# Performance work log

Hardware: AMD Instinct MI355X
Metric: run time of the kernel (lower is better)

Reference implementation:

```python
import jax, jax.numpy as jnp
import numpy as np

PATCH = 3
SIGMA2 = 0.5 ** 2
EPS = 1e-8


def _gauss_kernel():
    # depthwise Gaussian patch kernel, shape (6, 1, P, P, P), normalized to sum 1
    c = (PATCH - 1) / 2.0
    zz, yy, xx = np.meshgrid(np.arange(PATCH), np.arange(PATCH), np.arange(PATCH), indexing='ij')
    d2 = (xx - c) ** 2 + (yy - c) ** 2 + (zz - c) ** 2
    g = np.exp(-d2 / SIGMA2).astype(np.float32)
    g /= g.sum()
    k = np.zeros((6, 1, PATCH, PATCH, PATCH), np.float32)
    k[:, 0] = g
    return jnp.asarray(k)


def _shift(x, axis, step):
    # zero-padded shift: step=+1 -> out[i] = x[i+1]; step=-1 -> out[i] = x[i-1]
    n = x.shape[axis]
    pad = [(0, 0)] * x.ndim
    lo = 1 if step > 0 else 0
    pad[axis] = (0, 1) if step > 0 else (1, 0)
    xp = jnp.pad(x, pad)
    idx = [slice(None)] * x.ndim
    idx[axis] = slice(lo, lo + n)
    return xp[tuple(idx)]


def _mind(img):
    # shift-conv (one-hot 3x3x3 kernels) == 6 axis shifts: +z,-z,+y,-y,+x,-x
    shifted = jnp.concatenate([
        _shift(img, 2, 1), _shift(img, 2, -1),
        _shift(img, 3, 1), _shift(img, 3, -1),
        _shift(img, 4, 1), _shift(img, 4, -1),
    ], axis=1)                                  # (B,6,D,H,W)
    diff2 = (shifted - img) ** 2                # broadcast over channel dim
    gk = _gauss_kernel()
    Dp = jax.lax.conv_general_dilated(
        diff2, gk, window_strides=(1, 1, 1), padding='SAME',
        feature_group_count=6,
        dimension_numbers=('NCDHW', 'OIDHW', 'NCDHW'))  # depthwise Gaussian smoothing
    Vx = Dp.mean(axis=1, keepdims=True)
    num = jnp.exp(-Dp / (Vx + EPS))
    return num / (num.sum(axis=1, keepdims=True) + EPS)


def setup_inputs() -> dict:
    key = jax.random.key(0)
    img = jax.random.normal(key, (2, 1, 192, 192, 192), dtype=jnp.float32)
    return {"img": img}


def reference(img):
    return _mind(img)
```

## Files before the change

### kernel.cpp

```cpp
#include <hip/hip_runtime.h>

#define DHW   192
#define DHW2  (DHW*DHW)
#define TX    64
#define TTY   4
#define YB    4
#define BY    (TTY*YB)
#define ZCH   16
#define NT    (TX*TTY)
#define RY    (BY+4)
#define RXW   (TX+8)
#define SLICE (RY*RXW)
#define NF4   (SLICE/4)
#define ROWF4 (RXW/4)

__global__ __launch_bounds__(NT)
void mind3d_kernel(const float* __restrict__ img, float* __restrict__ out)
{
    __shared__ float ring[4][SLICE];

    const int lane = threadIdx.x;
    const int ty   = threadIdx.y;
    const int tid  = ty*TX + lane;

    const int x0 = blockIdx.x * TX;
    const int y0 = blockIdx.y * BY;
    const int zi = blockIdx.z;
    const int nzc = DHW / ZCH;
    const int b  = zi / nzc;
    const int z0 = (zi - b*nzc) * ZCH;

    const float* imgb = img + (size_t)b * ((size_t)DHW * DHW2);

    const float a1 = 0.01831563889245986f;
    const float n1 = 1.0f/(1.0f + 2.0f*a1);
    const float norm3 = n1*n1*n1;

    const int gx = x0 + lane;
    const float mL = (gx == 0)     ? 0.f : 1.f;
    const float mR = (gx == DHW-1) ? 0.f : 1.f;
    const int wy = y0 + ty*YB;
    const int u  = lane + 4;

    auto load_slice = [&](int z) {
        float4* dst = (float4*)ring[(z + 8) & 3];
        if ((unsigned)z >= (unsigned)DHW) {
            for (int g = tid; g < NF4; g += NT)
                dst[g] = float4{0.f, 0.f, 0.f, 0.f};
        } else {
            const float* sp = imgb + (size_t)z * DHW2;
            for (int g = tid; g < NF4; g += NT) {
                int row = g / ROWF4;
                int c4  = g - row*ROWF4;
                int gy  = y0 - 2 + row;
                int gxs = x0 - 16/4*4 + (c4 << 2) + (16/4*4 - 4);
                float4 v = {0.f, 0.f, 0.f, 0.f};
                if ((unsigned)gy < (unsigned)DHW && (unsigned)gxs <= (unsigned)(DHW - 4))
                    v = *(const float4*)(sp + (size_t)gy*DHW + gxs);
                dst[g] = v;
            }
        }
    };

    float zm[YB][6], zc[YB][6];
    #pragma unroll
    for (int j = 0; j < YB; ++j)
        #pragma unroll
        for (int c = 0; c < 6; ++c) { zm[j][c] = 0.f; zc[j][c] = 0.f; }

    load_slice(z0 - 2);
    load_slice(z0 - 1);
    load_slice(z0);
    __syncthreads();

    for (int zs = z0 - 1; zs <= z0 + ZCH; ++zs) {
        if (zs < z0 + ZCH) load_slice(zs + 2);

        const bool zok = ((unsigned)zs < (unsigned)DHW);
        const float* rcs = ring[(zs + 8) & 3] + ty*YB*RXW + u;
        const float* rps = ring[(zs + 9) & 3] + (ty*YB + 1)*RXW + u;
        const float* rms = ring[(zs + 7) & 3] + (ty*YB + 1)*RXW + u;

        float A0,A1,A2,A3,A4, B0,B1,B2,B3,B4;
        A0 = rcs[-2];     A1 = rcs[-1];     A2 = rcs[0];   A3 = rcs[1];     A4 = rcs[2];
        B0 = rcs[RXW-2];  B1 = rcs[RXW-1];  B2 = rcs[RXW]; B3 = rcs[RXW+1]; B4 = rcs[RXW+2];

        float T[3][6];
        const int zcout = zs - 1;
        const bool emitz = (zcout >= z0);

        #pragma unroll
        for (int k = 0; k < 6; ++k) {
            const int gr = wy - 1 + k;
            const float* rk = rcs + (k + 2)*RXW;
            float C0 = rk[-2], C1 = rk[-1], C2 = rk[0], C3 = rk[1], C4 = rk[2];
            const float* pk = rps + k*RXW;
            const float* mk = rms + k*RXW;
            float zpL = pk[-1], zpC = pk[0], zpR = pk[1];
            float zmL = mk[-1], zmC = mk[0], zmR = mk[1];

            const bool rok = zok && ((unsigned)gr < (unsigned)DHW);
            if (rok) {
                float d0 = B1-B0, d1 = B2-B1, d2 = B3-B2, d3 = B4-B3;
                float q0 = d0*d0, q1 = d1*d1, q2 = d2*d2, q3 = d3*d3;
                float eL, eC, eR;
                eL = zpL-B1; eC = zpC-B2; eR = zpR-B3;
                T[k%3][0] = a1*(eL*eL*mL + eR*eR*mR) + eC*eC;
                eL = zmL-B1; eC = zmC-B2; eR = zmR-B3;
                T[k%3][1] = a1*(eL*eL*mL + eR*eR*mR) + eC*eC;
                eL = C1-B1;  eC = C2-B2;  eR = C3-B3;
                T[k%3][2] = a1*(eL*eL*mL + eR*eR*mR) + eC*eC;
                eL = A1-B1;  eC = A2-B2;  eR = A3-B3;
                T[k%3][3] = a1*(eL*eL*mL + eR*eR*mR) + eC*eC;
                T[k%3][4] = a1*(q1*mL + q3*mR) + q2;
                T[k%3][5] = a1*(q0*mL + q2*mR) + q1;
            } else {
                #pragma unroll
                for (int c = 0; c < 6; ++c) T[k%3][c] = 0.f;
            }

            if (k >= 2) {
                const int j = k - 2;
                float sp_[6];
                #pragma unroll
                for (int c = 0; c < 6; ++c)
                    sp_[c] = a1*(T[(k-2)%3][c] + T[k%3][c]) + T[(k-1)%3][c];
                if (emitz) {
                    float dp[6], sum = 0.f;
                    #pragma unroll
                    for (int c = 0; c < 6; ++c) {
                        dp[c] = norm3 * (a1*(zm[j][c] + sp_[c]) + zc[j][c]);
                        sum += dp[c];
                    }
                    float inv = 1.0f / (sum * (1.0f/6.0f) + 1e-8f);
                    float num[6], nsum = 0.f;
                    #pragma unroll
                    for (int c = 0; c < 6; ++c) {
                        num[c] = __expf(-dp[c] * inv);
                        nsum += num[c];
                    }
                    float rs = 1.0f / (nsum + 1e-8f);
                    size_t base = ((size_t)(6*b)*DHW + zcout) * (size_t)DHW2
                                + (size_t)(wy + j)*DHW + (size_t)gx;
                    #pragma unroll
                    for (int c = 0; c < 6; ++c)
                        out[base + (size_t)c * ((size_t)DHW*DHW2)] = num[c]*rs;
                }
                #pragma unroll
                for (int c = 0; c < 6; ++c) { zm[j][c] = zc[j][c]; zc[j][c] = sp_[c]; }
            }
            A0=B0; A1=B1; A2=B2; A3=B3; A4=B4;
            B0=C0; B1=C1; B2=C2; B3=C3; B4=C4;
        }
        __syncthreads();
    }
}

extern "C" void kernel_launch(void* const* d_in, const int* in_sizes, int n_in,
                              void* d_out, int out_size, void* d_ws, size_t ws_size,
                              hipStream_t stream)
{
    const float* img = (const float*)d_in[0];
    float* out = (float*)d_out;
    dim3 block(TX, TTY, 1);
    dim3 grid(DHW/TX, DHW/BY, 2*(DHW/ZCH));
    hipLaunchKernelGGL(mind3d_kernel, grid, block, 0, stream, img, out);
}
```

Baseline: 423.0 us.

## Reuse +z smoothed channel as next slice's -z, prefetch slices into registers, halve z-chunk

Exploits the symmetry between the +z and -z squared-difference channels. The 2D-smoothed +z term from the previous slice is carried in registers and reused as the -z term for the current slice, so -z is computed directly only on the warm-up slice. Slice loads are split into a global-to-register issue one iteration ahead and a later commit to shared memory, which hides load latency behind compute. The z-chunk is halved to create more blocks and launch bounds request 4 waves per EU. In exchange, each chunk recomputes more halo slices and the carried state raises register pressure.

```diff
diff --git a/kernel.cpp b/kernel.cpp
--- a/kernel.cpp
+++ b/kernel.cpp
@@ -6,7 +6,7 @@
 #define TTY   4
 #define YB    4
 #define BY    (TTY*YB)
-#define ZCH   16
+#define ZCH   8
 #define NT    (TX*TTY)
 #define RY    (BY+4)
 #define RXW   (TX+8)
@@ -14,7 +14,7 @@
 #define NF4   (SLICE/4)
 #define ROWF4 (RXW/4)
 
-__global__ __launch_bounds__(NT)
+__global__ __launch_bounds__(NT, 4)
 void mind3d_kernel(const float* __restrict__ img, float* __restrict__ out)
 {
     __shared__ float ring[4][SLICE];
@@ -42,48 +42,57 @@
     const int wy = y0 + ty*YB;
     const int u  = lane + 4;
 
-    auto load_slice = [&](int z) {
-        float4* dst = (float4*)ring[(z + 8) & 3];
-        if ((unsigned)z >= (unsigned)DHW) {
-            for (int g = tid; g < NF4; g += NT)
-                dst[g] = float4{0.f, 0.f, 0.f, 0.f};
-        } else {
+    const int r0  = tid / ROWF4, c0i = tid - r0*ROWF4;
+    const int gy0s = y0 - 2 + r0, gx0s = x0 - 4 + (c0i << 2);
+    const bool in0 = ((unsigned)gy0s < (unsigned)DHW) && ((unsigned)gx0s <= (unsigned)(DHW-4));
+    const int t2  = tid + NT;
+    const bool g2 = (t2 < NF4);
+    const int r1  = t2 / ROWF4, c1i = t2 - r1*ROWF4;
+    const int gy1s = y0 - 2 + r1, gx1s = x0 - 4 + (c1i << 2);
+    const bool in1 = g2 && ((unsigned)gy1s < (unsigned)DHW) && ((unsigned)gx1s <= (unsigned)(DHW-4));
+
+    float4 sv0, sv1;
+    auto issue = [&](int z) {
+        sv0 = float4{0.f,0.f,0.f,0.f};
+        sv1 = float4{0.f,0.f,0.f,0.f};
+        if ((unsigned)z < (unsigned)DHW) {
             const float* sp = imgb + (size_t)z * DHW2;
-            for (int g = tid; g < NF4; g += NT) {
-                int row = g / ROWF4;
-                int c4  = g - row*ROWF4;
-                int gy  = y0 - 2 + row;
-                int gxs = x0 - 16/4*4 + (c4 << 2) + (16/4*4 - 4);
-                float4 v = {0.f, 0.f, 0.f, 0.f};
-                if ((unsigned)gy < (unsigned)DHW && (unsigned)gxs <= (unsigned)(DHW - 4))
-                    v = *(const float4*)(sp + (size_t)gy*DHW + gxs);
-                dst[g] = v;
-            }
+            if (in0) sv0 = *(const float4*)(sp + (size_t)gy0s*DHW + gx0s);
+            if (in1) sv1 = *(const float4*)(sp + (size_t)gy1s*DHW + gx1s);
         }
     };
+    auto commit = [&](int z) {
+        float4* dst = (float4*)ring[(z + 8) & 3];
+        dst[tid] = sv0;
+        if (g2) dst[t2] = sv1;
+    };
 
-    float zm[YB][6], zc[YB][6];
+    float zm[YB][6], zc[YB][6], zS0[YB];
     #pragma unroll
-    for (int j = 0; j < YB; ++j)
+    for (int j = 0; j < YB; ++j) {
+        zS0[j] = 0.f;
         #pragma unroll
         for (int c = 0; c < 6; ++c) { zm[j][c] = 0.f; zc[j][c] = 0.f; }
+    }
 
-    load_slice(z0 - 2);
-    load_slice(z0 - 1);
-    load_slice(z0);
+    issue(z0-2); commit(z0-2);
+    issue(z0-1); commit(z0-1);
+    issue(z0);   commit(z0);
+    issue(z0+1);
     __syncthreads();
 
     for (int zs = z0 - 1; zs <= z0 + ZCH; ++zs) {
-        if (zs < z0 + ZCH) load_slice(zs + 2);
+        if (zs + 2 <= z0 + ZCH + 1) commit(zs + 2);
+        if (zs + 3 <= z0 + ZCH + 1) issue(zs + 3);
 
-        const bool zok = ((unsigned)zs < (unsigned)DHW);
+        const bool zok  = ((unsigned)zs < (unsigned)DHW);
+        const bool warm = (zs == z0 - 1);
         const float* rcs = ring[(zs + 8) & 3] + ty*YB*RXW + u;
         const float* rps = ring[(zs + 9) & 3] + (ty*YB + 1)*RXW + u;
         const float* rms = ring[(zs + 7) & 3] + (ty*YB + 1)*RXW + u;
 
-        float A0,A1,A2,A3,A4, B0,B1,B2,B3,B4;
-        A0 = rcs[-2];     A1 = rcs[-1];     A2 = rcs[0];   A3 = rcs[1];     A4 = rcs[2];
-        B0 = rcs[RXW-2];  B1 = rcs[RXW-1];  B2 = rcs[RXW]; B3 = rcs[RXW+1]; B4 = rcs[RXW+2];
+        float A1 = rcs[-1], A2 = rcs[0], A3 = rcs[1];
+        float B0 = rcs[RXW-2], B1 = rcs[RXW-1], B2 = rcs[RXW], B3 = rcs[RXW+1], B4 = rcs[RXW+2];
 
         float T[3][6];
         const int zcout = zs - 1;
@@ -95,36 +104,53 @@
             const float* rk = rcs + (k + 2)*RXW;
             float C0 = rk[-2], C1 = rk[-1], C2 = rk[0], C3 = rk[1], C4 = rk[2];
             const float* pk = rps + k*RXW;
-            const float* mk = rms + k*RXW;
             float zpL = pk[-1], zpC = pk[0], zpR = pk[1];
-            float zmL = mk[-1], zmC = mk[0], zmR = mk[1];
 
-            const bool rok = zok && ((unsigned)gr < (unsigned)DHW);
+            const bool rowok = ((unsigned)gr < (unsigned)DHW);
+            const bool rok   = zok && rowok;
+            float* Tk = T[k % 3];
+
+            {
+                float eL = zpL-B1, eC = zpC-B2, eR = zpR-B3;
+                Tk[0] = rowok ? (a1*(eL*eL*mL + eR*eR*mR) + eC*eC) : 0.f;
+            }
             if (rok) {
                 float d0 = B1-B0, d1 = B2-B1, d2 = B3-B2, d3 = B4-B3;
                 float q0 = d0*d0, q1 = d1*d1, q2 = d2*d2, q3 = d3*d3;
                 float eL, eC, eR;
-                eL = zpL-B1; eC = zpC-B2; eR = zpR-B3;
-                T[k%3][0] = a1*(eL*eL*mL + eR*eR*mR) + eC*eC;
-                eL = zmL-B1; eC = zmC-B2; eR = zmR-B3;
-                T[k%3][1] = a1*(eL*eL*mL + eR*eR*mR) + eC*eC;
                 eL = C1-B1;  eC = C2-B2;  eR = C3-B3;
-                T[k%3][2] = a1*(eL*eL*mL + eR*eR*mR) + eC*eC;
+                Tk[2] = a1*(eL*eL*mL + eR*eR*mR) + eC*eC;
                 eL = A1-B1;  eC = A2-B2;  eR = A3-B3;
-                T[k%3][3] = a1*(eL*eL*mL + eR*eR*mR) + eC*eC;
-                T[k%3][4] = a1*(q1*mL + q3*mR) + q2;
-                T[k%3][5] = a1*(q0*mL + q2*mR) + q1;
+                Tk[3] = a1*(eL*eL*mL + eR*eR*mR) + eC*eC;
+                Tk[4] = a1*(q1*mL + q3*mR) + q2;
+                Tk[5] = a1*(q0*mL + q2*mR) + q1;
             } else {
-                #pragma unroll
-                for (int c = 0; c < 6; ++c) T[k%3][c] = 0.f;
+                Tk[2]=0.f; Tk[3]=0.f; Tk[4]=0.f; Tk[5]=0.f;
+            }
+            if (warm) {
+                float t1v = 0.f;
+                if (rok) {
+                    const float* mk = rms + k*RXW;
+                    float zmL = mk[-1], zmC = mk[0], zmR = mk[1];
+                    float eL = zmL-B1, eC = zmC-B2, eR = zmR-B3;
+                    t1v = a1*(eL*eL*mL + eR*eR*mR) + eC*eC;
+                }
+                Tk[1] = t1v;
             }
 
             if (k >= 2) {
                 const int j = k - 2;
-                float sp_[6];
-                #pragma unroll
-                for (int c = 0; c < 6; ++c)
-                    sp_[c] = a1*(T[(k-2)%3][c] + T[k%3][c]) + T[(k-1)%3][c];
+                float s0 = a1*(T[(k-2)%3][0] + T[k%3][0]) + T[(k-1)%3][0];
+                float s2 = a1*(T[(k-2)%3][2] + T[k%3][2]) + T[(k-1)%3][2];
+                float s3 = a1*(T[(k-2)%3][3] + T[k%3][3]) + T[(k-1)%3][3];
+                float s4 = a1*(T[(k-2)%3][4] + T[k%3][4]) + T[(k-1)%3][4];
+                float s5 = a1*(T[(k-2)%3][5] + T[k%3][5]) + T[(k-1)%3][5];
+                float s1 = warm ? (a1*(T[(k-2)%3][1] + T[k%3][1]) + T[(k-1)%3][1])
+                                : (zok ? zS0[j] : 0.f);
+                zS0[j] = s0;
+                float s0st = zok ? s0 : 0.f;
+                float sp_[6] = {s0st, s1, s2, s3, s4, s5};
+
                 if (emitz) {
                     float dp[6], sum = 0.f;
                     #pragma unroll
@@ -149,7 +175,7 @@
                 #pragma unroll
                 for (int c = 0; c < 6; ++c) { zm[j][c] = zc[j][c]; zc[j][c] = sp_[c]; }
             }
-            A0=B0; A1=B1; A2=B2; A3=B3; A4=B4;
+            A1=B1; A2=B2; A3=B3;
             B0=C0; B1=C1; B2=C2; B3=C3; B4=C4;
         }
         __syncthreads();
```

Measured after the change: 410.2 us. 3.0% less time.
